# Performance work log

Hardware: AMD Instinct MI355X
Metric: run time of the kernel (lower is better)

## Reference

```python
import jax, jax.numpy as jnp
import numpy as np

B, S, D, H = 2, 2048, 128, 8
HD = D // H  # 16


def setup_inputs() -> dict:
    key = jax.random.key(0)
    ks = jax.random.split(key, 12)
    rnd = lambda k, sh, sc=1.0: jax.random.normal(k, sh, dtype=jnp.float32) * sc
    uni = lambda k, sh: jax.random.uniform(k, sh, dtype=jnp.float32) * 0.1  # scaled to keep softmax unsaturated
    return dict(
        x_tgt=rnd(ks[0], (B, S, D)),
        enc_out=rnd(ks[1], (B, S, D)),
        self_wq=uni(ks[2], (D, D)),
        self_wk=uni(ks[3], (D, D)),
        self_wv=uni(ks[4], (D, D)),
        cross_wq=uni(ks[5], (D, D)),
        cross_wk=uni(ks[6], (D, D)),
        cross_wv=uni(ks[7], (D, D)),
        w1=rnd(ks[8], (D, D), 0.02), b1=jnp.zeros((D,), jnp.float32),
        w2=rnd(ks[9], (D, D), 0.02), b2=jnp.zeros((D,), jnp.float32),
        w3=rnd(ks[10], (D, 4 * D), 0.02), b3=jnp.zeros((4 * D,), jnp.float32),
        w4=rnd(ks[11], (4 * D, D), 0.02), b4=jnp.zeros((D,), jnp.float32),
        mask_src=jnp.ones((B, S), jnp.int32),
        mask_tgt=jnp.ones((B, S), jnp.int32),
    )


def _split(t):
    # faithful to torch: reshape (B,S,HD,H) then permute -> (B,H,S,HD)
    b, s, _ = t.shape
    return jnp.transpose(t.reshape(b, s, HD, H), (0, 3, 1, 2))


def _merge(t):
    # inverse: (B,H,S,HD) -> (B,S,HD,H) -> (B,S,D)
    b, _, s, _ = t.shape
    return jnp.transpose(t, (0, 2, 3, 1)).reshape(b, s, D)


def _attn(x_kv, x_q, wq, wk, wv):
    q = _split(x_q @ wq)   # (B,H,Sq,HD)
    k = _split(x_kv @ wk)  # (B,H,Sk,HD)
    v = _split(x_kv @ wv)
    scores = jnp.einsum('bhqd,bhkd->bhqk', q, k) / jnp.sqrt(jnp.float32(HD))
    p = jax.nn.softmax(scores, axis=-1)  # masked=True branch: no additive mask
    return _merge(jnp.einsum('bhqk,bhkd->bhqd', p, v))


def _layer_norm(x):
    # eps-less custom norm: (x - mean) / var, with unbiased variance (N-1)
    m = jnp.mean(x, axis=-1, keepdims=True)
    c = x - m
    var = jnp.sum(c * c, axis=-1, keepdims=True) / (D - 1)
    return c / var


def reference(x_tgt, enc_out, self_wq, self_wk, self_wv, cross_wq, cross_wk, cross_wv,
              w1, b1, w2, b2, w3, b3, w4, b4, mask_src, mask_tgt):
    # masked self-attention on target embeddings (no causal mask in source code)
    sa = _attn(x_tgt, x_tgt, self_wq, self_wk, self_wv)
    r1 = sa @ w1 + b1 + x_tgt
    # 'cross' attention: K/V from decoder input, Q from encoder output (faithful quirk)
    ca = _attn(x_tgt, enc_out, cross_wq, cross_wk, cross_wv)
    r2 = ca @ w2 + b2 + r1
    ln = _layer_norm(r2)
    h = jax.nn.relu(ln @ w3 + b3)
    return h @ w4 + b4 + r2
```

## Files before the change

### kernel.cpp

```cpp
#include <hip/hip_runtime.h>
#include <hip/hip_bf16.h>

#define BB 2
#define SS 2048
#define DD 128
#define HH 8
#define HDIM 16
#define DF 512
#define SPK 36
#define HS 520
#define LNS 136

typedef float floatx4 __attribute__((ext_vector_type(4)));
typedef float floatx16 __attribute__((ext_vector_type(16)));
typedef short frag8 __attribute__((ext_vector_type(8)));

__device__ __forceinline__ short f2bf(float x) {
  union { __hip_bfloat16 h; short s; } u;
  u.h = __float2bfloat16(x);
  return u.s;
}
__device__ __forceinline__ unsigned int pkbf(float a, float b) {
  float2 f; f.x = a; f.y = b;
  union { __hip_bfloat162 h2; unsigned int u; } u;
  u.h2 = __float22bfloat162_rn(f);
  return u.u;
}
__device__ __forceinline__ frag8 cvt8(const float4 a, const float4 b) {
  union { frag8 f; unsigned int u[4]; } x;
  x.u[0] = pkbf(a.x, a.y);
  x.u[1] = pkbf(a.z, a.w);
  x.u[2] = pkbf(b.x, b.y);
  x.u[3] = pkbf(b.z, b.w);
  return x.f;
}

struct WSrc { const float* p[10]; };
__global__ __launch_bounds__(256) void wprep_kernel(WSrc w, short* __restrict__ dst) {
  const int wi = blockIdx.y;
  const int kshift = (wi == 9) ? 9 : 7;
  const int N = (wi == 8) ? 512 : 128;
  const int total = N << kshift;
  const int offs[10] = {0, 16384, 32768, 49152, 65536, 81920, 98304, 114688, 131072, 196608};
  const float sc = (wi == 0 || wi == 3) ? 0.25f * 1.4426950408889634f : 1.0f;
  const float* src = w.p[wi];
  short* d = dst + offs[wi];
  const int K = 1 << kshift;
  for (int idx = blockIdx.x * 256 + threadIdx.x; idx < total; idx += gridDim.x * 256) {
    const int n = idx >> kshift, k = idx & (K - 1);
    d[idx] = f2bf(src[k * N + n] * sc);
  }
}

__global__ __launch_bounds__(64) void qkv_kernel(const float* __restrict__ x_tgt,
                                                 const float* __restrict__ enc_out,
                                                 const short* __restrict__ wt,
                                                 short* __restrict__ Qs, short* __restrict__ Ks,
                                                 short* __restrict__ Vts,
                                                 short* __restrict__ Qc, short* __restrict__ Kc,
                                                 short* __restrict__ Vtc) {
  const int lane = threadIdx.x, quad = lane >> 4, l16 = lane & 15;
  const int mbase = blockIdx.x * 16;
  const int which = blockIdx.y;
  const int kind = which % 3;
  const float* A = (which == 3) ? enc_out : x_tgt;
  const short* W = wt + which * 16384;
  short* Qb = (which < 3) ? Qs : Qc;
  short* Kb = (which < 3) ? Ks : Kc;
  short* Vtb = (which < 3) ? Vts : Vtc;

  __shared__ short sC[16 * 130];

  floatx4 acc[8];
#pragma unroll
  for (int ct = 0; ct < 8; ct++) acc[ct] = (floatx4){0.f, 0.f, 0.f, 0.f};

#pragma unroll
  for (int ks = 0; ks < 4; ks++) {
    const float4* ar = (const float4*)&A[(size_t)(mbase + l16) * DD + ks * 32 + quad * 8];
    const frag8 af = cvt8(ar[0], ar[1]);
#pragma unroll
    for (int ct = 0; ct < 8; ct++) {
      const frag8 bf = *(const frag8*)&W[(ct * 16 + l16) * DD + ks * 32 + quad * 8];
      acc[ct] = __builtin_amdgcn_mfma_f32_16x16x32_bf16(af, bf, acc[ct], 0, 0, 0);
    }
  }

#pragma unroll
  for (int ct = 0; ct < 8; ct++) {
#pragma unroll
    for (int r = 0; r < 4; r++) {
      sC[(quad * 4 + r) * 130 + ct * 16 + l16] = f2bf(acc[ct][r]);
    }
  }

  const int b = mbase >> 11;
  const int sbase = mbase & 2047;
  if (kind <= 1) {
    short* Dst = (kind == 0) ? Qb : Kb;
    const int s = lane >> 2, c4 = lane & 3;
#pragma unroll
    for (int h = 0; h < 8; h++) {
      short4 v;
      v.x = sC[s * 130 + (c4 * 4 + 0) * 8 + h];
      v.y = sC[s * 130 + (c4 * 4 + 1) * 8 + h];
      v.z = sC[s * 130 + (c4 * 4 + 2) * 8 + h];
      v.w = sC[s * 130 + (c4 * 4 + 3) * 8 + h];
      const int bh = b * HH + h;
      *(short4*)&Dst[((size_t)bh * SS + sbase + s) * HDIM + c4 * 4] = v;
    }
  } else {
    const int dci = lane >> 2, c4 = lane & 3;
#pragma unroll
    for (int h = 0; h < 8; h++) {
      short4 v;
      v.x = sC[(c4 * 4 + 0) * 130 + dci * 8 + h];
      v.y = sC[(c4 * 4 + 1) * 130 + dci * 8 + h];
      v.z = sC[(c4 * 4 + 2) * 130 + dci * 8 + h];
      v.w = sC[(c4 * 4 + 3) * 130 + dci * 8 + h];
      const int bh = b * HH + h;
      *(short4*)&Vtb[((size_t)bh * HDIM + dci) * SS + sbase + c4 * 4] = v;
    }
  }
}

__global__ __launch_bounds__(256) void attn_mfma_kernel(
    const short* __restrict__ Qa, const short* __restrict__ Ka,
    const short* __restrict__ Vta, short* __restrict__ AMa,
    const short* __restrict__ Qc, const short* __restrict__ Kc,
    const short* __restrict__ Vtc, short* __restrict__ AMc) {
  const int t = threadIdx.x, wid = t >> 6, lane = t & 63;
  const int l32 = lane & 31, half = lane >> 5;
  const int quad = (lane >> 4) & 3, l16 = lane & 15;
  const int bh = blockIdx.y;
  const int qbase = blockIdx.x * 32;
  const int inst = blockIdx.z;
  const short* Q = inst ? Qc : Qa;
  const short* K = inst ? Kc : Ka;
  const short* Vt = inst ? Vtc : Vta;
  short* AM = inst ? AMc : AMa;
  const size_t headoff = (size_t)bh * SS;

  __shared__ short sP[4][32 * SPK];
  __shared__ float pnum[4][16 * 33];
  __shared__ float pl[4][32];

  const frag8 qf = *(const frag8*)&Q[(headoff + qbase + l32) * HDIM + half * 8];

  frag8 onef;
#pragma unroll
  for (int i = 0; i < 8; i++) onef[i] = (short)0x3f80;

  floatx4 acc_o[2], acc_l[2];
  acc_o[0] = (floatx4){0.f, 0.f, 0.f, 0.f}; acc_o[1] = acc_o[0];
  acc_l[0] = acc_o[0]; acc_l[1] = acc_o[0];

  const int keyw = wid * 512;
#pragma unroll 1
  for (int it = 0; it < 16; it++) {
    const int kb = keyw + it * 32;
    const frag8 kf = *(const frag8*)&K[(headoff + kb + l32) * HDIM + half * 8];
    const floatx16 z16 = {0.f};
    const floatx16 sc = __builtin_amdgcn_mfma_f32_32x32x16_bf16(kf, qf, z16, 0, 0, 0);
#pragma unroll
    for (int g = 0; g < 4; g++) {
      const float e0 = __builtin_amdgcn_exp2f(sc[4 * g + 0]);
      const float e1 = __builtin_amdgcn_exp2f(sc[4 * g + 1]);
      const float e2 = __builtin_amdgcn_exp2f(sc[4 * g + 2]);
      const float e3 = __builtin_amdgcn_exp2f(sc[4 * g + 3]);
      uint2 pk;
      pk.x = pkbf(e0, e1);
      pk.y = pkbf(e2, e3);
      *(uint2*)&sP[wid][l32 * SPK + g * 8 + half * 4] = pk;
    }
#pragma unroll
    for (int qh = 0; qh < 2; qh++) {
      const frag8 pf = *(const frag8*)&sP[wid][(qh * 16 + l16) * SPK + quad * 8];
      const frag8 vf = *(const frag8*)&Vt[((size_t)bh * HDIM + l16) * SS + kb + quad * 8];
      acc_o[qh] = __builtin_amdgcn_mfma_f32_16x16x32_bf16(vf, pf, acc_o[qh], 0, 0, 0);
      acc_l[qh] = __builtin_amdgcn_mfma_f32_16x16x32_bf16(onef, pf, acc_l[qh], 0, 0, 0);
    }
  }

#pragma unroll
  for (int qh = 0; qh < 2; qh++) {
#pragma unroll
    for (int r = 0; r < 4; r++) {
      pnum[wid][(quad * 4 + r) * 33 + qh * 16 + l16] = acc_o[qh][r];
    }
    if (quad == 0) pl[wid][qh * 16 + l16] = acc_l[qh][0];
  }
  __syncthreads();

  {
    const int b = bh >> 3, h = bh & 7;
#pragma unroll
    for (int idx = t; idx < 512; idx += 256) {
      const int q16 = idx & 31, d = idx >> 5;
      const float num = pnum[0][d * 33 + q16] + pnum[1][d * 33 + q16] +
                        pnum[2][d * 33 + q16] + pnum[3][d * 33 + q16];
      const float l = pl[0][q16] + pl[1][q16] + pl[2][q16] + pl[3][q16];
      AM[((size_t)b * SS + qbase + q16) * DD + d * 8 + h] = f2bf(num / l);
    }
  }
}

__global__ __launch_bounds__(256) void tail_kernel(
    const short* __restrict__ AMs, const short* __restrict__ AMc,
    const short* __restrict__ W1, const short* __restrict__ W2,
    const float* __restrict__ b1, const float* __restrict__ b2,
    const float* __restrict__ x_tgt,
    const short* __restrict__ W3, const float* __restrict__ b3,
    const short* __restrict__ W4, const float* __restrict__ b4,
    float* __restrict__ Out) {
  const int t = threadIdx.x, w = t >> 6, lane = t & 63;
  const int quad = lane >> 4, l16 = lane & 15;
  const int mbase = blockIdx.x * 16;

  __shared__ float sumS[4][16];
  __shared__ float sumQ[4][16];
  __shared__ short sLN[16 * LNS];
  __shared__ short hs[16 * HS];

  floatx4 acc2[2];
  acc2[0] = (floatx4){0.f, 0.f, 0.f, 0.f};
  acc2[1] = (floatx4){0.f, 0.f, 0.f, 0.f};
#pragma unroll
  for (int ks = 0; ks < 4; ks++) {
    const frag8 afS = *(const frag8*)&AMs[(size_t)(mbase + l16) * DD + ks * 32 + quad * 8];
    const frag8 afC = *(const frag8*)&AMc[(size_t)(mbase + l16) * DD + ks * 32 + quad * 8];
#pragma unroll
    for (int c = 0; c < 2; c++) {
      const int n0 = (w * 2 + c) * 16 + l16;
      const frag8 bf1 = *(const frag8*)&W1[n0 * DD + ks * 32 + quad * 8];
      const frag8 bf2 = *(const frag8*)&W2[n0 * DD + ks * 32 + quad * 8];
      acc2[c] = __builtin_amdgcn_mfma_f32_16x16x32_bf16(afS, bf1, acc2[c], 0, 0, 0);
      acc2[c] = __builtin_amdgcn_mfma_f32_16x16x32_bf16(afC, bf2, acc2[c], 0, 0, 0);
    }
  }

  float v[2][4];
#pragma unroll
  for (int c = 0; c < 2; c++) {
    const int n = w * 32 + c * 16 + l16;
    const float bn = b1[n] + b2[n];
#pragma unroll
    for (int r = 0; r < 4; r++) {
      const int m = mbase + quad * 4 + r;
      v[c][r] = acc2[c][r] + bn + x_tgt[(size_t)m * DD + n];
    }
  }

#pragma unroll
  for (int r = 0; r < 4; r++) {
    float s = v[0][r] + v[1][r];
    float sq = v[0][r] * v[0][r] + v[1][r] * v[1][r];
#pragma unroll
    for (int mk = 1; mk < 16; mk <<= 1) {
      s += __shfl_xor(s, mk, 64);
      sq += __shfl_xor(sq, mk, 64);
    }
    if (l16 == 0) {
      sumS[w][quad * 4 + r] = s;
      sumQ[w][quad * 4 + r] = sq;
    }
  }
  __syncthreads();

#pragma unroll
  for (int r = 0; r < 4; r++) {
    const int row = quad * 4 + r;
    const float S = sumS[0][row] + sumS[1][row] + sumS[2][row] + sumS[3][row];
    const float Qs_ = sumQ[0][row] + sumQ[1][row] + sumQ[2][row] + sumQ[3][row];
    const float mean = S * (1.0f / 128.0f);
    const float cs = Qs_ - S * mean;
    const float ivar = 127.0f / cs;
#pragma unroll
    for (int c = 0; c < 2; c++) {
      const int n = w * 32 + c * 16 + l16;
      sLN[row * LNS + n] = f2bf((v[c][r] - mean) * ivar);
    }
  }
  __syncthreads();

  {
    floatx4 acc[8];
#pragma unroll
    for (int ct = 0; ct < 8; ct++) acc[ct] = (floatx4){0.f, 0.f, 0.f, 0.f};
    const int nblk = w * 128;
#pragma unroll
    for (int ks = 0; ks < 4; ks++) {
      const frag8 af = *(const frag8*)&sLN[l16 * LNS + ks * 32 + quad * 8];
#pragma unroll
      for (int ct = 0; ct < 8; ct++) {
        const frag8 bf = *(const frag8*)&W3[(size_t)(nblk + ct * 16 + l16) * DD + ks * 32 + quad * 8];
        acc[ct] = __builtin_amdgcn_mfma_f32_16x16x32_bf16(af, bf, acc[ct], 0, 0, 0);
      }
    }
#pragma unroll
    for (int ct = 0; ct < 8; ct++) {
      const int n = nblk + ct * 16 + l16;
      const float bn = b3[n];
#pragma unroll
      for (int r = 0; r < 4; r++) {
        hs[(quad * 4 + r) * HS + n] = f2bf(fmaxf(acc[ct][r] + bn, 0.f));
      }
    }
  }
  __syncthreads();

  {
    floatx4 acc[2];
    acc[0] = (floatx4){0.f, 0.f, 0.f, 0.f};
    acc[1] = (floatx4){0.f, 0.f, 0.f, 0.f};
#pragma unroll 4
    for (int ks = 0; ks < 16; ks++) {
      const frag8 af = *(const frag8*)&hs[l16 * HS + ks * 32 + quad * 8];
#pragma unroll
      for (int c = 0; c < 2; c++) {
        const int n0 = w * 32 + c * 16 + l16;
        const frag8 bf = *(const frag8*)&W4[(size_t)n0 * DF + ks * 32 + quad * 8];
        acc[c] = __builtin_amdgcn_mfma_f32_16x16x32_bf16(af, bf, acc[c], 0, 0, 0);
      }
    }
#pragma unroll
    for (int c = 0; c < 2; c++) {
      const int n = w * 32 + c * 16 + l16;
      const float bn = b4[n];
#pragma unroll
      for (int r = 0; r < 4; r++) {
        const int m = mbase + quad * 4 + r;
        Out[(size_t)m * DD + n] = acc[c][r] + bn + v[c][r];
      }
    }
  }
}

extern "C" void kernel_launch(void* const* d_in, const int* in_sizes, int n_in,
                              void* d_out, int out_size, void* d_ws, size_t ws_size,
                              hipStream_t stream) {
  (void)in_sizes; (void)n_in; (void)out_size; (void)ws_size;
  const float* x_tgt   = (const float*)d_in[0];
  const float* enc_out = (const float*)d_in[1];
  const float* b1 = (const float*)d_in[9];
  const float* b2 = (const float*)d_in[11];
  const float* b3 = (const float*)d_in[13];
  const float* b4 = (const float*)d_in[15];

  WSrc wsrc;
  wsrc.p[0] = (const float*)d_in[2];
  wsrc.p[1] = (const float*)d_in[3];
  wsrc.p[2] = (const float*)d_in[4];
  wsrc.p[3] = (const float*)d_in[5];
  wsrc.p[4] = (const float*)d_in[6];
  wsrc.p[5] = (const float*)d_in[7];
  wsrc.p[6] = (const float*)d_in[8];
  wsrc.p[7] = (const float*)d_in[10];
  wsrc.p[8] = (const float*)d_in[12];
  wsrc.p[9] = (const float*)d_in[14];

  float* ws = (float*)d_ws;
  short* wt   = (short*)(ws + 0);
  short* Qs   = (short*)(ws + 131072);
  short* Ks   = (short*)(ws + 393216);
  short* Vts  = (short*)(ws + 655360);
  short* AMs  = (short*)(ws + 917504);
  short* Qc   = (short*)(ws + 1179648);
  short* Kc   = (short*)(ws + 1441792);
  short* Vtc  = (short*)(ws + 1703936);
  short* AMc  = (short*)(ws + 1966080);

  const int M = BB * SS;
  const int MT = M / 16;

  wprep_kernel<<<dim3(64, 10), 256, 0, stream>>>(wsrc, wt);

  qkv_kernel<<<dim3(MT, 6), 64, 0, stream>>>(x_tgt, enc_out, wt, Qs, Ks, Vts, Qc, Kc, Vtc);

  attn_mfma_kernel<<<dim3(SS / 32, BB * HH, 2), 256, 0, stream>>>(
      Qs, Ks, Vts, AMs, Qc, Kc, Vtc, AMc);

  tail_kernel<<<MT, 256, 0, stream>>>(AMs, AMc, wt + 98304, wt + 114688,
                                      b1, b2, x_tgt, wt + 131072, b3,
                                      wt + 196608, b4, (float*)d_out);
}
```

Baseline: 147.8 us.

## Split QKV and tail kernels across more waves; double-buffer attention P tile

```diff
diff --git a/kernel.cpp b/kernel.cpp
--- a/kernel.cpp
+++ b/kernel.cpp
@@ -52,14 +52,15 @@
   }
 }
 
-__global__ __launch_bounds__(64) void qkv_kernel(const float* __restrict__ x_tgt,
-                                                 const float* __restrict__ enc_out,
-                                                 const short* __restrict__ wt,
-                                                 short* __restrict__ Qs, short* __restrict__ Ks,
-                                                 short* __restrict__ Vts,
-                                                 short* __restrict__ Qc, short* __restrict__ Kc,
-                                                 short* __restrict__ Vtc) {
-  const int lane = threadIdx.x, quad = lane >> 4, l16 = lane & 15;
+__global__ __launch_bounds__(128) void qkv_kernel(const float* __restrict__ x_tgt,
+                                                  const float* __restrict__ enc_out,
+                                                  const short* __restrict__ wt,
+                                                  short* __restrict__ Qs, short* __restrict__ Ks,
+                                                  short* __restrict__ Vts,
+                                                  short* __restrict__ Qc, short* __restrict__ Kc,
+                                                  short* __restrict__ Vtc) {
+  const int t = threadIdx.x, wv = t >> 6, lane = t & 63;
+  const int quad = lane >> 4, l16 = lane & 15;
   const int mbase = blockIdx.x * 16;
   const int which = blockIdx.y;
   const int kind = which % 3;
@@ -71,28 +72,30 @@
 
   __shared__ short sC[16 * 130];
 
-  floatx4 acc[8];
-#pragma unroll
-  for (int ct = 0; ct < 8; ct++) acc[ct] = (floatx4){0.f, 0.f, 0.f, 0.f};
+  floatx4 acc[4];
+#pragma unroll
+  for (int ci = 0; ci < 4; ci++) acc[ci] = (floatx4){0.f, 0.f, 0.f, 0.f};
 
 #pragma unroll
   for (int ks = 0; ks < 4; ks++) {
     const float4* ar = (const float4*)&A[(size_t)(mbase + l16) * DD + ks * 32 + quad * 8];
     const frag8 af = cvt8(ar[0], ar[1]);
 #pragma unroll
-    for (int ct = 0; ct < 8; ct++) {
+    for (int ci = 0; ci < 4; ci++) {
+      const int ct = wv * 4 + ci;
       const frag8 bf = *(const frag8*)&W[(ct * 16 + l16) * DD + ks * 32 + quad * 8];
-      acc[ct] = __builtin_amdgcn_mfma_f32_16x16x32_bf16(af, bf, acc[ct], 0, 0, 0);
-    }
-  }
-
-#pragma unroll
-  for (int ct = 0; ct < 8; ct++) {
+      acc[ci] = __builtin_amdgcn_mfma_f32_16x16x32_bf16(af, bf, acc[ci], 0, 0, 0);
+    }
+  }
+
+#pragma unroll
+  for (int ci = 0; ci < 4; ci++) {
 #pragma unroll
     for (int r = 0; r < 4; r++) {
-      sC[(quad * 4 + r) * 130 + ct * 16 + l16] = f2bf(acc[ct][r]);
-    }
-  }
+      sC[(quad * 4 + r) * 130 + (wv * 4 + ci) * 16 + l16] = f2bf(acc[ci][r]);
+    }
+  }
+  __syncthreads();
 
   const int b = mbase >> 11;
   const int sbase = mbase & 2047;
@@ -100,7 +103,8 @@
     short* Dst = (kind == 0) ? Qb : Kb;
     const int s = lane >> 2, c4 = lane & 3;
 #pragma unroll
-    for (int h = 0; h < 8; h++) {
+    for (int hh = 0; hh < 4; hh++) {
+      const int h = wv * 4 + hh;
       short4 v;
       v.x = sC[s * 130 + (c4 * 4 + 0) * 8 + h];
       v.y = sC[s * 130 + (c4 * 4 + 1) * 8 + h];
@@ -112,7 +116,8 @@
   } else {
     const int dci = lane >> 2, c4 = lane & 3;
 #pragma unroll
-    for (int h = 0; h < 8; h++) {
+    for (int hh = 0; hh < 4; hh++) {
+      const int h = wv * 4 + hh;
       short4 v;
       v.x = sC[(c4 * 4 + 0) * 130 + dci * 8 + h];
       v.y = sC[(c4 * 4 + 1) * 130 + dci * 8 + h];
@@ -141,9 +146,7 @@
   short* AM = inst ? AMc : AMa;
   const size_t headoff = (size_t)bh * SS;
 
-  __shared__ short sP[4][32 * SPK];
-  __shared__ float pnum[4][16 * 33];
-  __shared__ float pl[4][32];
+  __shared__ short sP[2][4][32 * SPK];
 
   const frag8 qf = *(const frag8*)&Q[(headoff + qbase + l32) * HDIM + half * 8];
 
@@ -156,9 +159,10 @@
   acc_l[0] = acc_o[0]; acc_l[1] = acc_o[0];
 
   const int keyw = wid * 512;
-#pragma unroll 1
+#pragma unroll 2
   for (int it = 0; it < 16; it++) {
     const int kb = keyw + it * 32;
+    short* sPw = &sP[it & 1][wid][0];
     const frag8 kf = *(const frag8*)&K[(headoff + kb + l32) * HDIM + half * 8];
     const floatx16 z16 = {0.f};
     const floatx16 sc = __builtin_amdgcn_mfma_f32_32x32x16_bf16(kf, qf, z16, 0, 0, 0);
@@ -171,24 +175,28 @@
       uint2 pk;
       pk.x = pkbf(e0, e1);
       pk.y = pkbf(e2, e3);
-      *(uint2*)&sP[wid][l32 * SPK + g * 8 + half * 4] = pk;
+      *(uint2*)&sPw[l32 * SPK + g * 8 + half * 4] = pk;
     }
 #pragma unroll
     for (int qh = 0; qh < 2; qh++) {
-      const frag8 pf = *(const frag8*)&sP[wid][(qh * 16 + l16) * SPK + quad * 8];
+      const frag8 pf = *(const frag8*)&sPw[(qh * 16 + l16) * SPK + quad * 8];
       const frag8 vf = *(const frag8*)&Vt[((size_t)bh * HDIM + l16) * SS + kb + quad * 8];
       acc_o[qh] = __builtin_amdgcn_mfma_f32_16x16x32_bf16(vf, pf, acc_o[qh], 0, 0, 0);
       acc_l[qh] = __builtin_amdgcn_mfma_f32_16x16x32_bf16(onef, pf, acc_l[qh], 0, 0, 0);
     }
   }
 
-#pragma unroll
-  for (int qh = 0; qh < 2; qh++) {
-#pragma unroll
-    for (int r = 0; r < 4; r++) {
-      pnum[wid][(quad * 4 + r) * 33 + qh * 16 + l16] = acc_o[qh][r];
-    }
-    if (quad == 0) pl[wid][qh * 16 + l16] = acc_l[qh][0];
+  {
+    float* pn = (float*)&sP[0][wid][0];
+    float* plw = (float*)&sP[1][wid][0];
+#pragma unroll
+    for (int qh = 0; qh < 2; qh++) {
+#pragma unroll
+      for (int r = 0; r < 4; r++) {
+        pn[(quad * 4 + r) * 33 + qh * 16 + l16] = acc_o[qh][r];
+      }
+      if (quad == 0) plw[qh * 16 + l16] = acc_l[qh][0];
+    }
   }
   __syncthreads();
 
@@ -197,15 +205,18 @@
 #pragma unroll
     for (int idx = t; idx < 512; idx += 256) {
       const int q16 = idx & 31, d = idx >> 5;
-      const float num = pnum[0][d * 33 + q16] + pnum[1][d * 33 + q16] +
-                        pnum[2][d * 33 + q16] + pnum[3][d * 33 + q16];
-      const float l = pl[0][q16] + pl[1][q16] + pl[2][q16] + pl[3][q16];
+      float num = 0.f, l = 0.f;
+#pragma unroll
+      for (int w = 0; w < 4; w++) {
+        num += ((const float*)&sP[0][w][0])[d * 33 + q16];
+        l += ((const float*)&sP[1][w][0])[q16];
+      }
       AM[((size_t)b * SS + qbase + q16) * DD + d * 8 + h] = f2bf(num / l);
     }
   }
 }
 
-__global__ __launch_bounds__(256) void tail_kernel(
+__global__ __launch_bounds__(512) void tail_kernel(
     const short* __restrict__ AMs, const short* __restrict__ AMc,
     const short* __restrict__ W1, const short* __restrict__ W2,
     const float* __restrict__ b1, const float* __restrict__ b2,
@@ -216,45 +227,38 @@
   const int t = threadIdx.x, w = t >> 6, lane = t & 63;
   const int quad = lane >> 4, l16 = lane & 15;
   const int mbase = blockIdx.x * 16;
-
-  __shared__ float sumS[4][16];
-  __shared__ float sumQ[4][16];
+  const int nA = w * 16 + l16;
+
+  __shared__ float sumS[8][16];
+  __shared__ float sumQ[8][16];
   __shared__ short sLN[16 * LNS];
   __shared__ short hs[16 * HS];
 
-  floatx4 acc2[2];
-  acc2[0] = (floatx4){0.f, 0.f, 0.f, 0.f};
-  acc2[1] = (floatx4){0.f, 0.f, 0.f, 0.f};
+  floatx4 acc2 = (floatx4){0.f, 0.f, 0.f, 0.f};
 #pragma unroll
   for (int ks = 0; ks < 4; ks++) {
     const frag8 afS = *(const frag8*)&AMs[(size_t)(mbase + l16) * DD + ks * 32 + quad * 8];
     const frag8 afC = *(const frag8*)&AMc[(size_t)(mbase + l16) * DD + ks * 32 + quad * 8];
-#pragma unroll
-    for (int c = 0; c < 2; c++) {
-      const int n0 = (w * 2 + c) * 16 + l16;
-      const frag8 bf1 = *(const frag8*)&W1[n0 * DD + ks * 32 + quad * 8];
-      const frag8 bf2 = *(const frag8*)&W2[n0 * DD + ks * 32 + quad * 8];
-      acc2[c] = __builtin_amdgcn_mfma_f32_16x16x32_bf16(afS, bf1, acc2[c], 0, 0, 0);
-      acc2[c] = __builtin_amdgcn_mfma_f32_16x16x32_bf16(afC, bf2, acc2[c], 0, 0, 0);
-    }
-  }
-
-  float v[2][4];
-#pragma unroll
-  for (int c = 0; c < 2; c++) {
-    const int n = w * 32 + c * 16 + l16;
-    const float bn = b1[n] + b2[n];
+    const frag8 bf1 = *(const frag8*)&W1[nA * DD + ks * 32 + quad * 8];
+    const frag8 bf2 = *(const frag8*)&W2[nA * DD + ks * 32 + quad * 8];
+    acc2 = __builtin_amdgcn_mfma_f32_16x16x32_bf16(afS, bf1, acc2, 0, 0, 0);
+    acc2 = __builtin_amdgcn_mfma_f32_16x16x32_bf16(afC, bf2, acc2, 0, 0, 0);
+  }
+
+  float v[4];
+  {
+    const float bn = b1[nA] + b2[nA];
 #pragma unroll
     for (int r = 0; r < 4; r++) {
       const int m = mbase + quad * 4 + r;
-      v[c][r] = acc2[c][r] + bn + x_tgt[(size_t)m * DD + n];
+      v[r] = acc2[r] + bn + x_tgt[(size_t)m * DD + nA];
     }
   }
 
 #pragma unroll
   for (int r = 0; r < 4; r++) {
-    float s = v[0][r] + v[1][r];
-    float sq = v[0][r] * v[0][r] + v[1][r] * v[1][r];
+    float s = v[r];
+    float sq = v[r] * v[r];
 #pragma unroll
     for (int mk = 1; mk < 16; mk <<= 1) {
       s += __shfl_xor(s, mk, 64);
@@ -270,68 +274,55 @@
 #pragma unroll
   for (int r = 0; r < 4; r++) {
     const int row = quad * 4 + r;
-    const float S = sumS[0][row] + sumS[1][row] + sumS[2][row] + sumS[3][row];
-    const float Qs_ = sumQ[0][row] + sumQ[1][row] + sumQ[2][row] + sumQ[3][row];
+    float S = 0.f, Qs_ = 0.f;
+#pragma unroll
+    for (int ww = 0; ww < 8; ww++) { S += sumS[ww][row]; Qs_ += sumQ[ww][row]; }
     const float mean = S * (1.0f / 128.0f);
     const float cs = Qs_ - S * mean;
     const float ivar = 127.0f / cs;
-#pragma unroll
-    for (int c = 0; c < 2; c++) {
-      const int n = w * 32 + c * 16 + l16;
-      sLN[row * LNS + n] = f2bf((v[c][r] - mean) * ivar);
-    }
-  }
-  __syncthreads();
-
-  {
-    floatx4 acc[8];
-#pragma unroll
-    for (int ct = 0; ct < 8; ct++) acc[ct] = (floatx4){0.f, 0.f, 0.f, 0.f};
-    const int nblk = w * 128;
+    sLN[row * LNS + nA] = f2bf((v[r] - mean) * ivar);
+  }
+  __syncthreads();
+
+  {
+    floatx4 acc[4];
+#pragma unroll
+    for (int ci = 0; ci < 4; ci++) acc[ci] = (floatx4){0.f, 0.f, 0.f, 0.f};
+    const int nblk = w * 64;
 #pragma unroll
     for (int ks = 0; ks < 4; ks++) {
       const frag8 af = *(const frag8*)&sLN[l16 * LNS + ks * 32 + quad * 8];
 #pragma unroll
-      for (int ct = 0; ct < 8; ct++) {
-        const frag8 bf = *(const frag8*)&W3[(size_t)(nblk + ct * 16 + l16) * DD + ks * 32 + quad * 8];
-        acc[ct] = __builtin_amdgcn_mfma_f32_16x16x32_bf16(af, bf, acc[ct], 0, 0, 0);
+      for (int ci = 0; ci < 4; ci++) {
+        const frag8 bf = *(const frag8*)&W3[(size_t)(nblk + ci * 16 + l16) * DD + ks * 32 + quad * 8];
+        acc[ci] = __builtin_amdgcn_mfma_f32_16x16x32_bf16(af, bf, acc[ci], 0, 0, 0);
       }
     }
 #pragma unroll
-    for (int ct = 0; ct < 8; ct++) {
-      const int n = nblk + ct * 16 + l16;
+    for (int ci = 0; ci < 4; ci++) {
+      const int n = nblk + ci * 16 + l16;
       const float bn = b3[n];
 #pragma unroll
       for (int r = 0; r < 4; r++) {
-        hs[(quad * 4 + r) * HS + n] = f2bf(fmaxf(acc[ct][r] + bn, 0.f));
+        hs[(quad * 4 + r) * HS + n] = f2bf(fmaxf(acc[ci][r] + bn, 0.f));
       }
     }
   }
   __syncthreads();
 
   {
-    floatx4 acc[2];
-    acc[0] = (floatx4){0.f, 0.f, 0.f, 0.f};
-    acc[1] = (floatx4){0.f, 0.f, 0.f, 0.f};
+    floatx4 acc = (floatx4){0.f, 0.f, 0.f, 0.f};
 #pragma unroll 4
     for (int ks = 0; ks < 16; ks++) {
       const frag8 af = *(const frag8*)&hs[l16 * HS + ks * 32 + quad * 8];
-#pragma unroll
-      for (int c = 0; c < 2; c++) {
-        const int n0 = w * 32 + c * 16 + l16;
-        const frag8 bf = *(const frag8*)&W4[(size_t)n0 * DF + ks * 32 + quad * 8];
-        acc[c] = __builtin_amdgcn_mfma_f32_16x16x32_bf16(af, bf, acc[c], 0, 0, 0);
-      }
-    }
-#pragma unroll
-    for (int c = 0; c < 2; c++) {
-      const int n = w * 32 + c * 16 + l16;
-      const float bn = b4[n];
-#pragma unroll
-      for (int r = 0; r < 4; r++) {
-        const int m = mbase + quad * 4 + r;
-        Out[(size_t)m * DD + n] = acc[c][r] + bn + v[c][r];
-      }
+      const frag8 bf = *(const frag8*)&W4[(size_t)nA * DF + ks * 32 + quad * 8];
+      acc = __builtin_amdgcn_mfma_f32_16x16x32_bf16(af, bf, acc, 0, 0, 0);
+    }
+    const float bn = b4[nA];
+#pragma unroll
+    for (int r = 0; r < 4; r++) {
+      const int m = mbase + quad * 4 + r;
+      Out[(size_t)m * DD + nA] = acc[r] + bn + v[r];
     }
   }
 }
@@ -375,12 +366,12 @@
 
   wprep_kernel<<<dim3(64, 10), 256, 0, stream>>>(wsrc, wt);
 
-  qkv_kernel<<<dim3(MT, 6), 64, 0, stream>>>(x_tgt, enc_out, wt, Qs, Ks, Vts, Qc, Kc, Vtc);
+  qkv_kernel<<<dim3(MT, 6), 128, 0, stream>>>(x_tgt, enc_out, wt, Qs, Ks, Vts, Qc, Kc, Vtc);
 
   attn_mfma_kernel<<<dim3(SS / 32, BB * HH, 2), 256, 0, stream>>>(
       Qs, Ks, Vts, AMs, Qc, Kc, Vtc, AMc);
 
-  tail_kernel<<<MT, 256, 0, stream>>>(AMs, AMc, wt + 98304, wt + 114688,
+  tail_kernel<<<MT, 512, 0, stream>>>(AMs, AMc, wt + 98304, wt + 114688,
                                       b1, b2, x_tgt, wt + 131072, b3,
                                       wt + 196608, b4, (float*)d_out);
 }
```

New measurement: 156.9 us. 6.1% more time.
